# Performance work log

Measured on AMD Instinct MI355X. Metric: run time of the kernel, lower is better.

Reference implementation:

```python
import jax, jax.numpy as jnp
import numpy as np

N_NODES = 20000
N_EDGES = 320000
N_FEAT = 128
N_CLASS = 10
NEG_SLOPE = 0.2  # PyG GATConv default LeakyReLU slope


def gat_conv(x, src, dst, ew, W, a_src, a_dst, b, heads, ch, concat):
    """PyG-style GATConv with multiplicative edge_weight on messages.
    x: [N, Fin]; src/dst: [E] (self-loops already included); ew: [E].
    """
    N = x.shape[0]
    h = (x @ W).reshape(N, heads, ch)                      # [N,H,C]
    al_s = jnp.sum(h * a_src, axis=-1)                     # [N,H]
    al_d = jnp.sum(h * a_dst, axis=-1)                     # [N,H]
    e = jax.nn.leaky_relu(al_s[src] + al_d[dst], NEG_SLOPE)  # [E,H]
    # segment softmax over incoming edges of each target node
    m = jax.ops.segment_max(e, dst, num_segments=N)        # [N,H]
    ex = jnp.exp(e - m[dst])
    den = jax.ops.segment_sum(ex, dst, num_segments=N)     # [N,H]
    alpha = ex / (den[dst] + 1e-16)                        # [E,H]
    msg = h[src] * (alpha * ew[:, None])[..., None]        # [E,H,C]
    out = jax.ops.segment_sum(msg, dst, num_segments=N)    # [N,H,C]
    out = out.reshape(N, heads * ch) if concat else out.mean(axis=1)
    return out + b


def setup_inputs() -> dict:
    key = jax.random.key(0)
    ks = jax.random.split(key, 20)
    d = {}
    d["x"] = jax.random.normal(ks[0], (N_NODES, N_FEAT), dtype=jnp.float32)
    d["edge_index"] = jax.random.randint(ks[1], (2, N_EDGES), 0, N_NODES, dtype=jnp.int32)
    d["edge_weight"] = jnp.ones((N_EDGES,), dtype=jnp.float32)

    def glorot(k, shape):
        fan = shape[0] + shape[-1]
        return jax.random.uniform(k, shape, jnp.float32, -1.0, 1.0) * np.sqrt(6.0 / fan)

    H1, C1 = 4, 256
    H3, C3 = 6, N_CLASS
    d["W1"] = glorot(ks[2], (N_FEAT, H1 * C1))
    d["a1s"] = glorot(ks[3], (H1, C1)) * 0.1
    d["a1d"] = glorot(ks[4], (H1, C1)) * 0.1
    d["b1"] = jnp.zeros((H1 * C1,), jnp.float32)
    d["lw1"] = glorot(ks[5], (N_FEAT, H1 * C1))
    d["lb1"] = jnp.zeros((H1 * C1,), jnp.float32)

    d["W2"] = glorot(ks[6], (H1 * C1, H1 * C1))
    d["a2s"] = glorot(ks[7], (H1, C1)) * 0.1
    d["a2d"] = glorot(ks[8], (H1, C1)) * 0.1
    d["b2"] = jnp.zeros((H1 * C1,), jnp.float32)
    d["lw2"] = glorot(ks[9], (H1 * C1, H1 * C1))
    d["lb2"] = jnp.zeros((H1 * C1,), jnp.float32)

    d["W3"] = glorot(ks[10], (H1 * C1, H3 * C3))
    d["a3s"] = glorot(ks[11], (H3, C3)) * 0.1
    d["a3d"] = glorot(ks[12], (H3, C3)) * 0.1
    d["b3"] = jnp.zeros((C3,), jnp.float32)
    d["lw3"] = glorot(ks[13], (H1 * C1, C3))
    d["lb3"] = jnp.zeros((C3,), jnp.float32)
    return d


def reference(x, edge_index, edge_weight,
              W1, a1s, a1d, b1, lw1, lb1,
              W2, a2s, a2d, b2, lw2, lb2,
              W3, a3s, a3d, b3, lw3, lb3):
    N = x.shape[0]
    # PyG GATConv adds self-loops (fill edge_weight with 1.0)
    loop = jnp.arange(N, dtype=edge_index.dtype)
    src = jnp.concatenate([edge_index[0], loop])
    dst = jnp.concatenate([edge_index[1], loop])
    ew = jnp.concatenate([edge_weight, jnp.ones((N,), edge_weight.dtype)])

    h = jax.nn.elu(gat_conv(x, src, dst, ew, W1, a1s, a1d, b1, 4, 256, True)
                   + (x @ lw1 + lb1))
    h = jax.nn.elu(gat_conv(h, src, dst, ew, W2, a2s, a2d, b2, 4, 256, True)
                   + (h @ lw2 + lb2))
    out = gat_conv(h, src, dst, ew, W3, a3s, a3d, b3, 6, N_CLASS, False) \
          + (h @ lw3 + lb3)
    return out
```

## Files before the change

kernel.cpp:

```cpp
#include <hip/hip_runtime.h>

typedef __attribute__((ext_vector_type(8))) short s16x8;
typedef __attribute__((ext_vector_type(8))) __bf16 bf16x8;
typedef __attribute__((ext_vector_type(4))) float f32x4;

__device__ inline float bf2f(ushort u){ return __uint_as_float(((unsigned)u)<<16); }
__device__ inline ushort f2bf(float f){
  unsigned u = __float_as_uint(f);
  unsigned r = (u + 0x7fffu + ((u>>16)&1u)) >> 16;
  return (ushort)r;
}

__device__ inline void gl_lds16(const ushort* g, ushort* l){
  __builtin_amdgcn_global_load_lds(
      (const __attribute__((address_space(1))) unsigned int*)g,
      (__attribute__((address_space(3))) unsigned int*)l,
      16, 0, 0);
}

__global__ void k_count(const int* __restrict__ ei, int* __restrict__ counts,
                        int E, int ET){
  int e = blockIdx.x*256 + threadIdx.x;
  if (e >= ET) return;
  int dst = (e < E) ? ei[E + e] : (e - E);
  atomicAdd(&counts[dst], 1);
}

__global__ __launch_bounds__(1024) void k_scan(const int* __restrict__ cnt,
                                               int* __restrict__ indptr, int N){
  __shared__ int part[1024];
  int t = threadIdx.x;
  int per = (N + 1023) / 1024;
  int base = t * per;
  int s = 0;
  for (int i = 0; i < per; ++i){ int idx = base + i; if (idx < N) s += cnt[idx]; }
  part[t] = s; __syncthreads();
  for (int off = 1; off < 1024; off <<= 1){
    int v = (t >= off) ? part[t-off] : 0;
    __syncthreads();
    if (t >= off) part[t] += v;
    __syncthreads();
  }
  int run = (t == 0) ? 0 : part[t-1];
  for (int i = 0; i < per; ++i){
    int idx = base + i;
    if (idx < N){ indptr[idx] = run; run += cnt[idx]; }
  }
  if (t == 1023) indptr[N] = run;
}

__global__ void k_fill(const int* __restrict__ ei, const float* __restrict__ ew,
                       const int* __restrict__ indptr, int* __restrict__ cursor,
                       int* __restrict__ csrc, float* __restrict__ cew,
                       int E, int ET){
  int e = blockIdx.x*256 + threadIdx.x;
  if (e >= ET) return;
  int src, dst; float w;
  if (e < E){ src = ei[e]; dst = ei[E + e]; w = ew[e]; }
  else { src = dst = e - E; w = 1.0f; }
  int pos = indptr[dst] + atomicAdd(&cursor[dst], 1);
  csrc[pos] = src; cew[pos] = w;
}

__global__ void k_f2b(const float* __restrict__ x, ushort* __restrict__ xb,
                      int n8valid, int n8total){
  int i = blockIdx.x*256 + threadIdx.x;
  if (i >= n8total) return;
  s16x8 o = {0,0,0,0,0,0,0,0};
  if (i < n8valid){
    const float4* p = (const float4*)x + (size_t)i*2;
    float4 a = p[0], b = p[1];
    o[0]=(short)f2bf(a.x); o[1]=(short)f2bf(a.y); o[2]=(short)f2bf(a.z); o[3]=(short)f2bf(a.w);
    o[4]=(short)f2bf(b.x); o[5]=(short)f2bf(b.y); o[6]=(short)f2bf(b.z); o[7]=(short)f2bf(b.w);
  }
  *((s16x8*)xb + i) = o;
}

__global__ __launch_bounds__(256) void k_packB(
    const float* __restrict__ W, const float* __restrict__ LW,
    ushort* __restrict__ BT, int K, int NW, int NL, int Npad)
{
  __shared__ float tile[32][33];
  int k0 = blockIdx.x*32, n0 = blockIdx.y*32;
  int c = threadIdx.x & 31, r4 = threadIdx.x >> 5;
  #pragma unroll
  for (int rr = 0; rr < 32; rr += 8){
    int k = k0 + r4 + rr, n = n0 + c;
    float v = 0.f;
    if (k < K){
      if (n < NW)            v = W[(size_t)k*NW + n];
      else if (n < NW + NL)  v = LW[(size_t)k*NL + (n - NW)];
    }
    tile[r4+rr][c] = v;
  }
  __syncthreads();
  #pragma unroll
  for (int rr = 0; rr < 32; rr += 8){
    int n = n0 + r4 + rr, k = k0 + c;
    if (n < Npad && k < K) BT[(size_t)n*K + k] = f2bf(tile[c][r4+rr]);
  }
}

__global__ __launch_bounds__(256) void k_gemm(
    const ushort* __restrict__ A, const ushort* __restrict__ BT,
    ushort* __restrict__ Gatt, ushort* __restrict__ Skip,
    int K, int GW, int SW, int NCB, int CPX)
{
  __shared__ ushort As[128*64];
  __shared__ ushort Bs[128*64];
  const int bid = blockIdx.x;
  const int lb = CPX ? ((bid & 7)*CPX + (bid >> 3)) : bid;
  const size_t row0 = (size_t)(lb / NCB) * 128;
  const size_t col0 = (size_t)(lb % NCB) * 128;
  const int t = threadIdx.x;
  const int l = t & 63, w = t >> 6;
  const int wr = w >> 1, wc = w & 1;
  const int sr = l >> 3;
  const int sk = ((l & 7) ^ sr) << 3;
  const ushort* gA = A  + (row0 + w*8 + sr)*(size_t)K + sk;
  const ushort* gB = BT + (col0 + w*8 + sr)*(size_t)K + sk;
  ushort* lA = As + w*512;
  ushort* lB = Bs + w*512;
  const int rf = l & 15;
  const int g4 = l >> 4;
  f32x4 acc[4][4] = {};

  for (int k0 = 0; k0 < K; k0 += 64){
    #pragma unroll
    for (int i = 0; i < 4; ++i){
      gl_lds16(gA + k0 + (size_t)(i*32)*K, lA + i*2048);
      gl_lds16(gB + k0 + (size_t)(i*32)*K, lB + i*2048);
    }
    __syncthreads();
    #pragma unroll
    for (int kk = 0; kk < 2; ++kk){
      const int koff = ((((kk<<2) | g4) ^ (rf & 7)) << 3);
      bf16x8 af[4], bfr[4];
      #pragma unroll
      for (int i = 0; i < 4; ++i)
        af[i] = __builtin_bit_cast(bf16x8, *(const s16x8*)(As + (wr*64 + i*16 + rf)*64 + koff));
      #pragma unroll
      for (int j = 0; j < 4; ++j)
        bfr[j] = __builtin_bit_cast(bf16x8, *(const s16x8*)(Bs + (wc*64 + j*16 + rf)*64 + koff));
      #pragma unroll
      for (int i = 0; i < 4; ++i)
        #pragma unroll
        for (int j = 0; j < 4; ++j)
          acc[i][j] = __builtin_amdgcn_mfma_f32_16x16x32_bf16(af[i], bfr[j], acc[i][j], 0, 0, 0);
    }
    __syncthreads();
  }

  #pragma unroll
  for (int i = 0; i < 4; ++i){
    #pragma unroll
    for (int j = 0; j < 4; ++j){
      int gc = (int)col0 + wc*64 + j*16 + rf;
      #pragma unroll
      for (int r = 0; r < 4; ++r){
        size_t gr = row0 + wr*64 + i*16 + (g4<<2) + r;
        float v = acc[i][j][r];
        if (gc < GW)            Gatt[gr*GW + gc] = f2bf(v);
        else if (gc < GW + SW)  Skip[gr*SW + (gc - GW)] = f2bf(v);
      }
    }
  }
}

#define STG8(p0, hh, ktv, offU) do { \
  const ushort* _g = (p0) + (((size_t)(hh))<<7)*(size_t)K + (((size_t)(ktv))<<6); \
  gl_lds16(_g, S + (offU) + (w<<9)); \
  gl_lds16(_g + ((size_t)K<<6), S + (offU) + 4096 + (w<<9)); \
} while(0)

#define RD_A(base_) do { _Pragma("unroll") \
  for (int i_ = 0; i_ < 4; ++i_){ \
    const int hr = wr*64 + i_*16 + rf; const int sw = hr & 7; \
    av[i_][0] = *(const bf16x8*)((base_) + hr*64 + ((g4 ^ sw) << 3)); \
    av[i_][1] = *(const bf16x8*)((base_) + hr*64 + (((4|g4) ^ sw) << 3)); } \
} while(0)

#define RD_B(base_, dst_) do { _Pragma("unroll") \
  for (int j_ = 0; j_ < 2; ++j_){ \
    const int cf = wc*32 + j_*16 + rf; const int sw = cf & 7; \
    dst_[j_][0] = *(const bf16x8*)((base_) + cf*64 + ((g4 ^ sw) << 3)); \
    dst_[j_][1] = *(const bf16x8*)((base_) + cf*64 + (((4|g4) ^ sw) << 3)); } \
} while(0)

#define MM8(mh, nh, bv_) do { \
  __builtin_amdgcn_s_setprio(1); \
  _Pragma("unroll") \
  for (int kk_ = 0; kk_ < 2; ++kk_) \
    _Pragma("unroll") \
    for (int i_ = 0; i_ < 4; ++i_) \
      _Pragma("unroll") \
      for (int j_ = 0; j_ < 2; ++j_) \
        acc[mh][nh][i_][j_] = __builtin_amdgcn_mfma_f32_16x16x32_bf16( \
            av[i_][kk_], bv_[j_][kk_], acc[mh][nh][i_][j_], 0, 0, 0); \
  __builtin_amdgcn_s_setprio(0); \
} while(0)

__global__ __launch_bounds__(512, 1) void k_gemm8(
    const ushort* __restrict__ A, const ushort* __restrict__ BT,
    ushort* __restrict__ Gatt, ushort* __restrict__ Skip,
    int K, int GW, int CPX)
{
  __shared__ ushort S[65536];
  const int bid = blockIdx.x;
  const int lb = (bid & 7)*CPX + (bid >> 3);
  const size_t row0 = (size_t)(lb >> 3) * 256;
  const size_t col0 = (size_t)(lb & 7) * 256;
  const int t = threadIdx.x;
  const int l = t & 63, w = t >> 6;
  const int wr = w >> 2, wc = w & 3;
  const int rf = l & 15, g4 = l >> 4;
  const int T = K >> 6;

  const int r0 = t >> 3, s0 = t & 7;
  const ushort* pA = A  + (row0 + r0)*(size_t)K + ((s0 ^ (r0 & 7)) << 3);
  const ushort* pB = BT + (col0 + r0)*(size_t)K + ((s0 ^ (r0 & 7)) << 3);

  f32x4 acc[2][2][4][2] = {};
  bf16x8 av[4][2], bvlo[2][2], bvhi[2][2];

  STG8(pA, 0, 0, 0);
  STG8(pB, 0, 0, 16384);
  STG8(pA, 1, 0, 8192);
  STG8(pB, 1, 0, 24576);
  STG8(pA, 0, 1, 32768);
  STG8(pB, 0, 1, 49152);
  asm volatile("s_waitcnt vmcnt(4)");
  asm volatile("s_barrier" ::: "memory");

  for (int u = 0; u < T; ++u){
    const int b = u & 1;
    const int bbase = b << 15;
    const int nbase = bbase ^ 32768;
    const bool un1 = (u + 1 < T), un2 = (u + 2 < T);
    const ushort* Alo = S + bbase;
    const ushort* Ahi = S + bbase + 8192;
    const ushort* Blo = S + bbase + 16384;
    const ushort* Bhi = S + bbase + 24576;
    RD_A(Alo); RD_B(Blo, bvlo);
    if (un1) STG8(pA, 1, u+1, nbase + 8192);
    MM8(0, 0, bvlo);
    asm volatile("s_barrier" ::: "memory");
    RD_B(Bhi, bvhi);
    if (un1) STG8(pB, 1, u+1, nbase + 24576);
    MM8(0, 1, bvhi);
    asm volatile("s_barrier" ::: "memory");
    RD_A(Ahi);
    if (un2) STG8(pA, 0, u+2, bbase);
    MM8(1, 1, bvhi);
    asm volatile("s_barrier" ::: "memory");
    if (un2) STG8(pB, 0, u+2, bbase + 16384);
    MM8(1, 0, bvlo);
    if (un2) asm volatile("s_waitcnt vmcnt(4)");
    else     asm volatile("s_waitcnt vmcnt(0)");
    asm volatile("s_barrier" ::: "memory");
  }

  ushort* outp; int cb;
  if ((int)col0 < GW){ outp = Gatt; cb = (int)col0; }
  else               { outp = Skip; cb = (int)col0 - GW; }
  #pragma unroll
  for (int mh = 0; mh < 2; ++mh)
    #pragma unroll
    for (int i = 0; i < 4; ++i)
      #pragma unroll
      for (int rr = 0; rr < 4; ++rr){
        size_t gr = row0 + mh*128 + wr*64 + i*16 + (g4<<2) + rr;
        ushort* rp = outp + gr*1024 + cb;
        #pragma unroll
        for (int nh = 0; nh < 2; ++nh)
          #pragma unroll
          for (int j = 0; j < 2; ++j)
            rp[nh*128 + wc*32 + j*16 + rf] = f2bf(acc[mh][nh][i][j][rr]);
      }
}

__global__ __launch_bounds__(256) void k_al(const ushort* __restrict__ Gatt,
    const float* __restrict__ a_s, const float* __restrict__ a_d,
    float* __restrict__ als, float* __restrict__ ald, int N){
  int gw = (blockIdx.x*blockDim.x + threadIdx.x) >> 6;
  int l = threadIdx.x & 63;
  if (gw >= N) return;
  const ushort* row = Gatt + (size_t)gw*1024;
  int c0 = l*16;
  s16x8 v0 = *(const s16x8*)(row + c0);
  s16x8 v1 = *(const s16x8*)(row + c0 + 8);
  float ps = 0.f, pd = 0.f;
  #pragma unroll
  for (int q = 0; q < 8; ++q){
    float f0 = bf2f((ushort)v0[q]), f1 = bf2f((ushort)v1[q]);
    ps += f0*a_s[c0+q] + f1*a_s[c0+8+q];
    pd += f0*a_d[c0+q] + f1*a_d[c0+8+q];
  }
  #pragma unroll
  for (int off = 8; off; off >>= 1){
    ps += __shfl_down(ps, off);
    pd += __shfl_down(pd, off);
  }
  if ((l & 15) == 0){
    als[(size_t)gw*4 + (l>>4)] = ps;
    ald[(size_t)gw*4 + (l>>4)] = pd;
  }
}

__global__ __launch_bounds__(256) void k_agg(
    const ushort* __restrict__ Gatt,
    const ushort* __restrict__ Skip,
    const float*  __restrict__ als,
    const float*  __restrict__ ald,
    const float*  __restrict__ bias,
    const float*  __restrict__ lbias,
    const int*    __restrict__ indptr,
    const int*    __restrict__ csrc,
    const float*  __restrict__ cew,
    ushort* __restrict__ Hout,
    int N)
{
  const int t = threadIdx.x;
  const int l = t & 63, w = t >> 6;
  const int n = blockIdx.x*4 + w;
  const int h2 = l >> 4;
  const int col = l*16;
  if (n >= N){
    s16x8 z = {0,0,0,0,0,0,0,0};
    *(s16x8*)(Hout + (size_t)n*1024 + col)     = z;
    *(s16x8*)(Hout + (size_t)n*1024 + col + 8) = z;
    return;
  }
  const int beg = indptr[n];
  const int deg = indptr[n+1] - beg;
  const int hh = l & 3;
  const float aldh = ald[(size_t)n*4 + hh];

  float m = -1e30f, d = 0.f;
  for (int c0 = 0; c0 < deg; c0 += 16){
    int i = c0 + (l >> 2);
    bool act = (i < deg);
    float e = -1e30f;
    if (act){
      int s = csrc[beg + i];
      float r_ = als[(size_t)s*4 + hh] + aldh;
      e = r_ > 0.f ? r_ : 0.2f*r_;
    }
    float cm = e;
    #pragma unroll
    for (int o = 4; o < 64; o <<= 1) cm = fmaxf(cm, __shfl_xor(cm, o));
    float nm = fmaxf(m, cm);
    float ex = act ? __expf(e - nm) : 0.f;
    #pragma unroll
    for (int o = 4; o < 64; o <<= 1) ex += __shfl_xor(ex, o);
    d = d * __expf(m - nm) + ex;
    m = nm;
  }
  d += 1e-16f;
  const float inv_d = 1.0f / d;

  float a[16];
  #pragma unroll
  for (int q = 0; q < 16; ++q) a[q] = 0.f;
  const ushort* gbase = Gatt + col;
  for (int c0 = 0; c0 < deg; c0 += 16){
    int i = c0 + (l >> 2);
    int nc = min(16, deg - c0);
    float wv = 0.f; int sv = 0;
    if (i < deg){
      sv = csrc[beg + i];
      float r_ = als[(size_t)sv*4 + hh] + aldh;
      float e = r_ > 0.f ? r_ : 0.2f*r_;
      wv = __expf(e - m) * inv_d * cew[beg + i];
    }
    for (int jj = 0; jj < nc; ++jj){
      float wg = __shfl(wv, (jj << 2) | h2);
      int s    = __shfl(sv, jj << 2);
      const ushort* rp = gbase + (size_t)s*1024;
      s16x8 h0 = *(const s16x8*)rp;
      s16x8 h1 = *(const s16x8*)(rp + 8);
      #pragma unroll
      for (int q = 0; q < 8; ++q) a[q]   += wg * bf2f((ushort)h0[q]);
      #pragma unroll
      for (int q = 0; q < 8; ++q) a[q+8] += wg * bf2f((ushort)h1[q]);
    }
  }

  s16x8 sk0 = *(const s16x8*)(Skip + (size_t)n*1024 + col);
  s16x8 sk1 = *(const s16x8*)(Skip + (size_t)n*1024 + col + 8);
  s16x8 ov0, ov1;
  #pragma unroll
  for (int q = 0; q < 8; ++q){
    float v = a[q] + bias[col+q] + lbias[col+q] + bf2f((ushort)sk0[q]);
    v = v > 0.f ? v : __expf(v) - 1.f;
    ov0[q] = (short)f2bf(v);
    float v2 = a[q+8] + bias[col+8+q] + lbias[col+8+q] + bf2f((ushort)sk1[q]);
    v2 = v2 > 0.f ? v2 : __expf(v2) - 1.f;
    ov1[q] = (short)f2bf(v2);
  }
  *(s16x8*)(Hout + (size_t)n*1024 + col)     = ov0;
  *(s16x8*)(Hout + (size_t)n*1024 + col + 8) = ov1;
}

__global__ void k_al3(const ushort* __restrict__ G3, const float* __restrict__ a_s,
                      const float* __restrict__ a_d,
                      float* __restrict__ als, float* __restrict__ ald, int N){
  int n = blockIdx.x*256 + threadIdx.x;
  if (n >= N) return;
  const ushort* row = G3 + (size_t)n*60;
  #pragma unroll
  for (int h = 0; h < 6; ++h){
    float ps = 0.f, pd = 0.f;
    #pragma unroll
    for (int c = 0; c < 10; ++c){
      float v = bf2f(row[h*10 + c]);
      ps += v * a_s[h*10 + c];
      pd += v * a_d[h*10 + c];
    }
    als[(size_t)n*6 + h] = ps;
    ald[(size_t)n*6 + h] = pd;
  }
}

__global__ __launch_bounds__(64) void k_agg3(
    const ushort* __restrict__ G3,
    const ushort* __restrict__ Skip3,
    const float*  __restrict__ als,
    const float*  __restrict__ ald,
    const float*  __restrict__ b3,
    const float*  __restrict__ lb3,
    const int*    __restrict__ indptr,
    const int*    __restrict__ csrc,
    const float*  __restrict__ cew,
    float* __restrict__ out, int N)
{
  const int n = blockIdx.x;
  const int l = threadIdx.x;
  const int beg = indptr[n], deg = indptr[n+1] - beg;
  __shared__ float s_aldh[6];
  __shared__ int   s_src[64];
  __shared__ float s_wgt[64][6];
  __shared__ float s_o[6][10];
  if (l < 6) s_aldh[l] = ald[(size_t)n*6 + l];
  __syncthreads();
  float m0=-1e30f,m1=-1e30f,m2=-1e30f,m3=-1e30f,m4=-1e30f,m5=-1e30f;
  float d0=0.f,d1=0.f,d2=0.f,d3=0.f,d4=0.f,d5=0.f;
  for (int c0 = 0; c0 < deg; c0 += 64){
    int nc = min(64, deg - c0);
    bool act = l < nc;
    int s = act ? csrc[beg + c0 + l] : 0;
#define HP(hh, mm, dd) { \
    float e = -1e30f; \
    if (act){ float r_ = als[(size_t)s*6 + hh] + s_aldh[hh]; e = r_ > 0.f ? r_ : 0.2f*r_; } \
    float cm = e; \
    for (int o_ = 32; o_; o_ >>= 1) cm = fmaxf(cm, __shfl_xor(cm, o_)); \
    float nm = fmaxf(mm, cm); \
    float ex = act ? __expf(e - nm) : 0.f; \
    for (int o_ = 32; o_; o_ >>= 1) ex += __shfl_xor(ex, o_); \
    dd = dd * __expf(mm - nm) + ex; mm = nm; }
    HP(0,m0,d0) HP(1,m1,d1) HP(2,m2,d2) HP(3,m3,d3) HP(4,m4,d4) HP(5,m5,d5)
#undef HP
  }
  const int h = l / 10, c = l % 10;
  float o = 0.f;
  for (int c0 = 0; c0 < deg; c0 += 64){
    int nc = min(64, deg - c0);
    if (l < nc){
      int s = csrc[beg + c0 + l];
      s_src[l] = s;
      float w_ = cew[beg + c0 + l];
#define WP(hh, mm, dd) { \
      float r_ = als[(size_t)s*6 + hh] + s_aldh[hh]; \
      float e = r_ > 0.f ? r_ : 0.2f*r_; \
      s_wgt[l][hh] = __expf(e - mm) / (dd + 1e-16f) * w_; }
      WP(0,m0,d0) WP(1,m1,d1) WP(2,m2,d2) WP(3,m3,d3) WP(4,m4,d4) WP(5,m5,d5)
#undef WP
    }
    __syncthreads();
    if (l < 60){
      for (int i = 0; i < nc; ++i)
        o += s_wgt[i][h] * bf2f(G3[(size_t)s_src[i]*60 + l]);
    }
    __syncthreads();
  }
  if (l < 60) s_o[h][c] = o;
  __syncthreads();
  if (l < 10){
    float v = (s_o[0][l]+s_o[1][l]+s_o[2][l]+s_o[3][l]+s_o[4][l]+s_o[5][l]) * (1.0f/6.0f);
    v += b3[l] + lb3[l] + bf2f(Skip3[(size_t)n*10 + l]);
    out[(size_t)n*10 + l] = v;
  }
}

extern "C" void kernel_launch(void* const* d_in, const int* in_sizes, int n_in,
                              void* d_out, int out_size, void* d_ws, size_t ws_size,
                              hipStream_t stream)
{
  const int N = 20000, F = 128, E = 320000, ET = E + N;
  const int Mpad = 20224;
  const int F1 = 1024, NT = 2048;
  const int NWG1 = (Mpad/128)*(NT/128);
  const int NWG2 = (Mpad/256)*(NT/256);

  const float* x   = (const float*)d_in[0];
  const int*   ei  = (const int*)  d_in[1];
  const float* ew  = (const float*)d_in[2];
  const float* W1  = (const float*)d_in[3];
  const float* a1s = (const float*)d_in[4];
  const float* a1d = (const float*)d_in[5];
  const float* b1  = (const float*)d_in[6];
  const float* lw1 = (const float*)d_in[7];
  const float* lb1 = (const float*)d_in[8];
  const float* W2  = (const float*)d_in[9];
  const float* a2s = (const float*)d_in[10];
  const float* a2d = (const float*)d_in[11];
  const float* b2  = (const float*)d_in[12];
  const float* lw2 = (const float*)d_in[13];
  const float* lb2 = (const float*)d_in[14];
  const float* W3  = (const float*)d_in[15];
  const float* a3s = (const float*)d_in[16];
  const float* a3d = (const float*)d_in[17];
  const float* b3  = (const float*)d_in[18];
  const float* lw3 = (const float*)d_in[19];
  const float* lb3 = (const float*)d_in[20];

  char* ws = (char*)d_ws;
  size_t off = 0;
  auto alloc = [&](size_t bytes) -> void* {
    void* p = ws + off;
    off = (off + bytes + 255) & ~(size_t)255;
    return p;
  };
  ushort* Gatt = (ushort*)alloc((size_t)Mpad*F1*2);
  ushort* Skip = (ushort*)alloc((size_t)Mpad*F1*2);
  ushort* H    = (ushort*)alloc((size_t)Mpad*F1*2);
  ushort* xb   = (ushort*)alloc((size_t)Mpad*F*2);
  ushort* BT   = (ushort*)alloc((size_t)NT*1024*2);
  float*  als  = (float*) alloc((size_t)N*6*4);
  float*  ald  = (float*) alloc((size_t)N*6*4);
  int*    counts = (int*)alloc((size_t)2*N*4);
  int*    cursor = counts + N;
  int*    indptr = (int*)alloc((size_t)(N+1)*4);
  int*    csrc   = (int*)alloc((size_t)ET*4);
  float*  cew    = (float*)alloc((size_t)ET*4);
  if (off > ws_size) return;

  hipMemsetAsync(counts, 0, (size_t)2*N*4, stream);
  k_count<<<(ET+255)/256, 256, 0, stream>>>(ei, counts, E, ET);
  k_scan<<<1, 1024, 0, stream>>>(counts, indptr, N);
  k_fill<<<(ET+255)/256, 256, 0, stream>>>(ei, ew, indptr, cursor, csrc, cew, E, ET);
  k_f2b<<<(Mpad*F/8+255)/256, 256, 0, stream>>>(x, xb, N*F/8, Mpad*F/8);

  k_packB<<<dim3((F+31)/32, NT/32), 256, 0, stream>>>(W1, lw1, BT, F, 1024, 1024, NT);
  k_gemm<<<dim3(NWG1), 256, 0, stream>>>(xb, BT, Gatt, Skip, F, 1024, 1024, NT/128, NWG1/8);
  k_al<<<(N+3)/4, 256, 0, stream>>>(Gatt, a1s, a1d, als, ald, N);
  k_agg<<<Mpad/4, 256, 0, stream>>>(Gatt, Skip, als, ald, b1, lb1, indptr, csrc, cew, H, N);

  k_packB<<<dim3(F1/32, NT/32), 256, 0, stream>>>(W2, lw2, BT, F1, 1024, 1024, NT);
  k_gemm8<<<dim3(NWG2), 512, 0, stream>>>(H, BT, Gatt, Skip, F1, 1024, NWG2/8);
  k_al<<<(N+3)/4, 256, 0, stream>>>(Gatt, a2s, a2d, als, ald, N);
  k_agg<<<Mpad/4, 256, 0, stream>>>(Gatt, Skip, als, ald, b2, lb2, indptr, csrc, cew, H, N);

  k_packB<<<dim3(F1/32, 128/32), 256, 0, stream>>>(W3, lw3, BT, F1, 60, 10, 128);
  k_gemm<<<dim3(Mpad/128), 256, 0, stream>>>(H, BT, Gatt, Skip, F1, 60, 10, 1, 0);
  k_al3<<<(N+255)/256, 256, 0, stream>>>(Gatt, a3s, a3d, als, ald, N);
  k_agg3<<<N, 64, 0, stream>>>(Gatt, Skip, als, ald, b3, lb3, indptr, csrc, cew,
                               (float*)d_out, N);
}
```

Baseline: 501.6 us.

## Split-K the layer-3 GEMM and unroll aggregation gather by two

```diff
diff --git a/kernel.cpp b/kernel.cpp
--- a/kernel.cpp
+++ b/kernel.cpp
@@ -165,6 +165,82 @@
       }
     }
   }
+}
+
+__global__ __launch_bounds__(256) void k_gemm_sk(
+    const ushort* __restrict__ A, const ushort* __restrict__ BT,
+    float* __restrict__ P, int K, int kseg, int Mpad)
+{
+  __shared__ ushort As[128*64];
+  __shared__ ushort Bs[128*64];
+  const int bid = blockIdx.x;
+  const int part = bid & 3;
+  const size_t row0 = (size_t)(bid >> 2) * 128;
+  const int kbeg = part * kseg;
+  const int kend = kbeg + kseg;
+  const int t = threadIdx.x;
+  const int l = t & 63, w = t >> 6;
+  const int wr = w >> 1, wc = w & 1;
+  const int sr = l >> 3;
+  const int sk = ((l & 7) ^ sr) << 3;
+  const ushort* gA = A  + (row0 + w*8 + sr)*(size_t)K + sk;
+  const ushort* gB = BT + (w*8 + sr)*(size_t)K + sk;
+  ushort* lA = As + w*512;
+  ushort* lB = Bs + w*512;
+  const int rf = l & 15;
+  const int g4 = l >> 4;
+  f32x4 acc[4][4] = {};
+
+  for (int k0 = kbeg; k0 < kend; k0 += 64){
+    #pragma unroll
+    for (int i = 0; i < 4; ++i){
+      gl_lds16(gA + k0 + (size_t)(i*32)*K, lA + i*2048);
+      gl_lds16(gB + k0 + (size_t)(i*32)*K, lB + i*2048);
+    }
+    __syncthreads();
+    #pragma unroll
+    for (int kk = 0; kk < 2; ++kk){
+      const int koff = ((((kk<<2) | g4) ^ (rf & 7)) << 3);
+      bf16x8 af[4], bfr[4];
+      #pragma unroll
+      for (int i = 0; i < 4; ++i)
+        af[i] = __builtin_bit_cast(bf16x8, *(const s16x8*)(As + (wr*64 + i*16 + rf)*64 + koff));
+      #pragma unroll
+      for (int j = 0; j < 4; ++j)
+        bfr[j] = __builtin_bit_cast(bf16x8, *(const s16x8*)(Bs + (wc*64 + j*16 + rf)*64 + koff));
+      #pragma unroll
+      for (int i = 0; i < 4; ++i)
+        #pragma unroll
+        for (int j = 0; j < 4; ++j)
+          acc[i][j] = __builtin_amdgcn_mfma_f32_16x16x32_bf16(af[i], bfr[j], acc[i][j], 0, 0, 0);
+    }
+    __syncthreads();
+  }
+
+  float* Pp = P + (size_t)part * Mpad * 128;
+  #pragma unroll
+  for (int i = 0; i < 4; ++i){
+    #pragma unroll
+    for (int j = 0; j < 4; ++j){
+      int gc = wc*64 + j*16 + rf;
+      #pragma unroll
+      for (int r = 0; r < 4; ++r){
+        size_t gr = row0 + wr*64 + i*16 + (g4<<2) + r;
+        Pp[gr*128 + gc] = acc[i][j][r];
+      }
+    }
+  }
+}
+
+__global__ void k_red3(const float* __restrict__ P, ushort* __restrict__ G3,
+                       ushort* __restrict__ S3, int Mpad){
+  int idx = blockIdx.x*256 + threadIdx.x;
+  int row = idx >> 7, gc = idx & 127;
+  if (row >= Mpad || gc >= 70) return;
+  const size_t st = (size_t)Mpad*128;
+  float v = P[idx] + P[idx+st] + P[idx+2*st] + P[idx+3*st];
+  if (gc < 60) G3[(size_t)row*60 + gc] = f2bf(v);
+  else         S3[(size_t)row*10 + (gc-60)] = f2bf(v);
 }
 
 #define STG8(p0, hh, ktv, offU) do { \
@@ -373,16 +449,35 @@
       float e = r_ > 0.f ? r_ : 0.2f*r_;
       wv = __expf(e - m) * inv_d * cew[beg + i];
     }
-    for (int jj = 0; jj < nc; ++jj){
+    int jj = 0;
+    for (; jj + 1 < nc; jj += 2){
+      float wg0 = __shfl(wv, (jj << 2) | h2);
+      int   sg0 = __shfl(sv, jj << 2);
+      float wg1 = __shfl(wv, ((jj+1) << 2) | h2);
+      int   sg1 = __shfl(sv, (jj+1) << 2);
+      const ushort* rp0 = gbase + (size_t)sg0*1024;
+      const ushort* rp1 = gbase + (size_t)sg1*1024;
+      s16x8 x0 = *(const s16x8*)rp0;
+      s16x8 x1 = *(const s16x8*)(rp0 + 8);
+      s16x8 y0 = *(const s16x8*)rp1;
+      s16x8 y1 = *(const s16x8*)(rp1 + 8);
+      #pragma unroll
+      for (int q = 0; q < 8; ++q){
+        a[q]   += wg0 * bf2f((ushort)x0[q]) + wg1 * bf2f((ushort)y0[q]);
+        a[q+8] += wg0 * bf2f((ushort)x1[q]) + wg1 * bf2f((ushort)y1[q]);
+      }
+    }
+    if (jj < nc){
       float wg = __shfl(wv, (jj << 2) | h2);
-      int s    = __shfl(sv, jj << 2);
+      int   s  = __shfl(sv, jj << 2);
       const ushort* rp = gbase + (size_t)s*1024;
       s16x8 h0 = *(const s16x8*)rp;
       s16x8 h1 = *(const s16x8*)(rp + 8);
       #pragma unroll
-      for (int q = 0; q < 8; ++q) a[q]   += wg * bf2f((ushort)h0[q]);
-      #pragma unroll
-      for (int q = 0; q < 8; ++q) a[q+8] += wg * bf2f((ushort)h1[q]);
+      for (int q = 0; q < 8; ++q){
+        a[q]   += wg * bf2f((ushort)h0[q]);
+        a[q+8] += wg * bf2f((ushort)h1[q]);
+      }
     }
   }
 
@@ -536,6 +631,7 @@
   ushort* H    = (ushort*)alloc((size_t)Mpad*F1*2);
   ushort* xb   = (ushort*)alloc((size_t)Mpad*F*2);
   ushort* BT   = (ushort*)alloc((size_t)NT*1024*2);
+  float*  P    = (float*) alloc((size_t)4*Mpad*128*4);
   float*  als  = (float*) alloc((size_t)N*6*4);
   float*  ald  = (float*) alloc((size_t)N*6*4);
   int*    counts = (int*)alloc((size_t)2*N*4);
@@ -562,7 +658,8 @@
   k_agg<<<Mpad/4, 256, 0, stream>>>(Gatt, Skip, als, ald, b2, lb2, indptr, csrc, cew, H, N);
 
   k_packB<<<dim3(F1/32, 128/32), 256, 0, stream>>>(W3, lw3, BT, F1, 60, 10, 128);
-  k_gemm<<<dim3(Mpad/128), 256, 0, stream>>>(H, BT, Gatt, Skip, F1, 60, 10, 1, 0);
+  k_gemm_sk<<<dim3((Mpad/128)*4), 256, 0, stream>>>(H, BT, P, F1, F1/4, Mpad);
+  k_red3<<<(Mpad*128)/256, 256, 0, stream>>>(P, Gatt, Skip, Mpad);
   k_al3<<<(N+255)/256, 256, 0, stream>>>(Gatt, a3s, a3d, als, ald, N);
   k_agg3<<<N, 64, 0, stream>>>(Gatt, Skip, als, ald, b3, lb3, indptr, csrc, cew,
                                (float*)d_out, N);
```

Result: no change. 499.6 us (-0.4%).
